# Optimization experiments

Hardware: AMD Instinct MI355X
Metric: run time of the kernel (lower is better)

Reference implementation:

```python
import jax, jax.numpy as jnp
import numpy as np
from jax import lax

TAU = 1.0
GUMBEL_SCALE = 1e-4
SEARCH_SPACE = [1, 2, 4, 8, 16, 32, 64]


def synth_weight(weight, alphas_after):
    """Per-block circulant projection of weight for each block size, mixed by alphas.

    weight: [O, I, k, k]. For block size b: reshape to (q,b,p,b,k,k), rotate rows so
    each circulant diagonal aligns, mean over the block row axis, broadcast back with
    the reverse rotation, and accumulate alpha-weighted.
    """
    O, I, k, _ = weight.shape
    w = alphas_after[0] * weight  # block_size == 1 -> identity
    for idx, b in enumerate(SEARCH_SPACE[1:], start=1):
        q, p = O // b, I // b
        tmp = weight.reshape(q, b, p, b, k, k).transpose(0, 2, 1, 3, 4, 5)  # q,p,b,b,k,k
        ii = jnp.arange(b)[:, None]
        jj = jnp.arange(b)[None, :]
        rot = tmp[:, :, ii, (ii + jj) % b]          # q,p,b,b,k,k : rotate_mat gather
        cir = rot.mean(axis=2)                       # q,p,b,k,k   : circulant mean
        out = cir[:, :, (jj - ii) % b]               # q,p,b,b,k,k : rev_rotate_mat gather
        out = out.transpose(0, 2, 1, 3, 4, 5).reshape(O, I, k, k)
        w = w + alphas_after[idx] * out
    return w


def setup_inputs() -> dict:
    key = jax.random.key(0)
    k1, k2, k3 = jax.random.split(key, 3)
    B, C, H = 16, 256, 56
    O, I, K = 256, 256, 3
    x = jax.random.normal(k1, (B, C, H, H), dtype=jnp.float32)
    # kaiming-uniform-ish init: uniform in [-bound, bound], bound = sqrt(6/fan_in)
    fan_in = I * K * K
    bound = float(np.sqrt(6.0 / fan_in))
    weight = jax.random.uniform(k2, (O, I, K, K), dtype=jnp.float32, minval=-bound, maxval=bound)
    alphas = jnp.ones((len(SEARCH_SPACE),), dtype=jnp.float32)
    gumbels = jax.random.normal(k3, (len(SEARCH_SPACE),), dtype=jnp.float32)
    return {"x": x, "weight": weight, "alphas": alphas, "gumbels": gumbels}


def reference(x, weight, alphas, gumbels):
    # gumbel_softmax with tiny Gumbel(0, 1e-4) noise (noise passed in for determinism)
    alphas_after = jax.nn.softmax((alphas + GUMBEL_SCALE * gumbels) / TAU, axis=-1)
    w = synth_weight(weight, alphas_after)
    k = weight.shape[-1]
    pad = k // 2
    stride = 1
    out = lax.conv_general_dilated(
        x, w,
        window_strides=(stride, stride),
        padding=[(pad, pad), (pad, pad)],
        dimension_numbers=("NCHW", "OIHW", "NCHW"),
    )
    return out
```

## Files before the change

kernel.cpp:

```cpp
#include <hip/hip_runtime.h>
#include <hip/hip_bf16.h>

typedef __attribute__((ext_vector_type(8))) short bf16x8;
typedef __attribute__((ext_vector_type(4))) float f32x4;

#define WR_OFF   27557888

#define BAND 24576

__global__ void diagsum_kernel(const float* __restrict__ W, float* __restrict__ S) {
    int t = blockIdx.x * 256 + threadIdx.x;
    int idx, n, lvlOff;
    if (t < 32768)      { idx = 1; n = t;          lvlOff = 0; }
    else if (t < 49152) { idx = 2; n = t - 32768;  lvlOff = 294912; }
    else if (t < 57344) { idx = 3; n = t - 49152;  lvlOff = 442368; }
    else if (t < 61440) { idx = 4; n = t - 57344;  lvlOff = 516096; }
    else if (t < 63488) { idx = 5; n = t - 61440;  lvlOff = 552960; }
    else                { idx = 6; n = t - 63488;  lvlOff = 571392; }
    int b = 1 << idx;
    int d = n & (b - 1);
    int qp = n >> idx;
    int p = qp & ((256 >> idx) - 1);
    int q = qp >> (8 - idx);
    float s[9];
    #pragma unroll
    for (int tp = 0; tp < 9; ++tp) s[tp] = 0.f;
    for (int tt = 0; tt < b; ++tt) {
        const float* wp = W + ((size_t)((q * b + tt) * 256 + p * b + ((tt + d) & (b - 1)))) * 9;
        #pragma unroll
        for (int tp = 0; tp < 9; ++tp) s[tp] += wp[tp];
    }
    float* o = S + (size_t)lvlOff + (size_t)n * 9;
    #pragma unroll
    for (int tp = 0; tp < 9; ++tp) o[tp] = s[tp];
}

__global__ void wsynth_kernel(const float* __restrict__ W,
                              const float* __restrict__ alphas,
                              const float* __restrict__ gumbels,
                              const float* __restrict__ S,
                              __hip_bfloat16* __restrict__ Wr) {
    int tid = blockIdx.x * 256 + threadIdx.x;
    int o = tid >> 8, i = tid & 255;

    float a[7]; float mx = -1e30f;
    for (int j = 0; j < 7; ++j) { a[j] = alphas[j] + 1.0e-4f * gumbels[j]; mx = fmaxf(mx, a[j]); }
    float s = 0.f;
    for (int j = 0; j < 7; ++j) { a[j] = __expf(a[j] - mx); s += a[j]; }
    float invs = 1.0f / s;
    for (int j = 0; j < 7; ++j) a[j] *= invs;

    float acc[9];
    const float* w0 = W + ((size_t)(o * 256 + i)) * 9;
    #pragma unroll
    for (int t = 0; t < 9; ++t) acc[t] = a[0] * w0[t];

    const int lvlOff[7] = {0, 0, 294912, 442368, 516096, 552960, 571392};
    int dif = i - o;
    #pragma unroll
    for (int idx = 1; idx < 7; ++idx) {
        int b = 1 << idx;
        int q = o >> idx, p = i >> idx, d = dif & (b - 1);
        int n = ((q * (256 >> idx) + p) << idx) + d;
        const float* sp = S + lvlOff[idx] + (size_t)n * 9;
        float sc = a[idx] / (float)b;
        #pragma unroll
        for (int tp = 0; tp < 9; ++tp) acc[tp] += sc * sp[tp];
    }
    const size_t eb = (size_t)(i >> 5) * 8192 + ((i >> 3) & 3) * 2048 + o * 8 + (i & 7);
    #pragma unroll
    for (int tp = 0; tp < 9; ++tp)
        Wr[(size_t)tp * 65536 + eb] = __float2bfloat16(acc[tp]);
}

__global__ void pad_nhwc_kernel(const float* __restrict__ x,
                                __hip_bfloat16* __restrict__ Xp) {
    {
        int bl = (blockIdx.z * 4 + blockIdx.y) * 49 + blockIdx.x;
        int L = bl * 256 + threadIdx.x;
        for (int e = L; e < 933888; e += 802816) {
            int c = e & 255;
            int pp = e >> 8;
            int b = pp / 228;
            int p = pp - b * 228;
            int y, xx;
            if (p < 58)       { y = 0;             xx = p; }
            else if (p < 116) { y = 57;            xx = p - 58; }
            else if (p < 172) { y = 1 + (p - 116); xx = 0; }
            else              { y = 1 + (p - 172); xx = 57; }
            Xp[((size_t)(b * 58 + y) * 58 + xx) * 256 + c] = __float2bfloat16(0.f);
        }
    }
    __shared__ float t[64][65];
    int p0 = blockIdx.x * 64;
    int c0 = blockIdx.y * 64;
    int b  = blockIdx.z;
    int lane = threadIdx.x & 63;
    int grp  = threadIdx.x >> 6;

    const float* src = x + ((size_t)(b * 256 + c0)) * 3136 + p0;
    #pragma unroll
    for (int it = 0; it < 16; ++it) {
        int c = it * 4 + grp;
        t[c][lane] = src[(size_t)c * 3136 + lane];
    }
    __syncthreads();
    #pragma unroll
    for (int it = 0; it < 16; ++it) {
        int pl = it * 4 + grp;
        int P = p0 + pl;
        int y = P / 56, xx = P - y * 56;
        Xp[(((size_t)(b * 58 + y + 1)) * 58 + (xx + 1)) * 256 + c0 + lane] =
            __float2bfloat16(t[lane][pl]);
    }
}

__device__ __forceinline__ void gload16(const __hip_bfloat16* g, char* l) {
    __builtin_amdgcn_global_load_lds(
        (const __attribute__((address_space(1))) void*)g,
        (__attribute__((address_space(3))) void*)l, 16, 0, 0);
}

template<int N> __device__ __forceinline__ void gate() {
    if constexpr (N == 0)      asm volatile("s_waitcnt vmcnt(0)" ::: "memory");
    else if constexpr (N == 4) asm volatile("s_waitcnt vmcnt(4)" ::: "memory");
}

template<bool LAST>
__device__ __forceinline__ void chunk_pair(
    int cp, char* smem, const char* aBase,
    const int (&bOff)[7], const __hip_bfloat16* const (&xSrc)[3],
    int tid, bf16x8 (&afr)[2][4], bf16x8 (&bfv)[2][7], f32x4 (&acc)[4][7])
{
    #pragma unroll
    for (int u = 0; u < 2; ++u) {
        const int cc = 2 * cp + u;
        const char* xb = smem + u * BAND;
        #pragma unroll
        for (int r = 0; r < 9; ++r) {
            const int cur = (u + r) & 1, nxt = cur ^ 1;
            if (r == 0 && !(LAST && u == 1)) {
                char* d = smem + (u ^ 1) * BAND + tid * 16;
                #pragma unroll
                for (int it = 0; it < 3; ++it)
                    gload16(xSrc[it] + (cc + 1) * 32, d + it * 8192);
            }
            if (!(LAST && u == 1 && r == 8)) {
                const int tapn = (r == 8) ? 0 : r + 1;
                const int aoff = tapn * 131072 + (cc + (r == 8 ? 1 : 0)) * 16384;
                #pragma unroll
                for (int nf = 0; nf < 4; ++nf)
                    afr[nxt][nf] = *(const bf16x8*)(aBase + aoff + nf * 256);
            }
            if (r < 8) {
                const int tapn = r + 1;
                const int timn = ((tapn / 3 - 1) * 64 + (tapn % 3 - 1)) * 16;
                #pragma unroll
                for (int mf = 0; mf < 7; ++mf)
                    bfv[nxt][mf] = *(const bf16x8*)(xb + bOff[mf] + timn);
            } else if (!(LAST && u == 1)) {
                const int timn = (-64 - 1) * 16;
                const char* xb2 = smem + (u ^ 1) * BAND;
                #pragma unroll
                for (int mf = 0; mf < 7; ++mf)
                    bfv[nxt][mf] = *(const bf16x8*)(xb2 + bOff[mf] + timn);
            }
            __builtin_amdgcn_sched_barrier(0);
            __builtin_amdgcn_s_setprio(1);
            #pragma unroll
            for (int nf = 0; nf < 4; ++nf)
                #pragma unroll
                for (int mf = 0; mf < 7; ++mf)
                    acc[nf][mf] = __builtin_amdgcn_mfma_f32_16x16x32_bf16(
                        afr[cur][nf], bfv[cur][mf], acc[nf][mf], 0, 0, 0);
            __builtin_amdgcn_s_setprio(0);
            if (r == 7 && !(LAST && u == 1)) {
                gate<4>();
                __builtin_amdgcn_s_barrier();
            }
        }
    }
}

__global__ __launch_bounds__(512, 2) void conv_kernel(
        const __hip_bfloat16* __restrict__ Xp,
        const __hip_bfloat16* __restrict__ Wr,
        float* __restrict__ out) {
    __shared__ char smem[2 * BAND];

    const int tid = threadIdx.x;
    const int w = tid >> 6, lane = tid & 63, l15 = lane & 15, q = lane >> 4;
    const int bid = blockIdx.x;
    const int bimg = bid / 14;
    const int y0 = (bid - bimg * 14) * 4;

    const int wn = (w & 3) << 6;
    const int wm = (w >> 2) * 112;

    const char* aBase = (const char*)Wr + q * 4096 + (wn + l15) * 16;

    const __hip_bfloat16* xSrc[3];
    #pragma unroll
    for (int it = 0; it < 3; ++it) {
        int chunk = tid + it * 512;
        int slot = chunk / 384;
        int rem  = chunk - slot * 384;
        int row = rem >> 6, xcol = rem & 63;
        xSrc[it] = Xp + (((size_t)(bimg * 58 + y0 + row)) * 58 + xcol) * 256 + slot * 8;
    }

    int bOff[7];
    #pragma unroll
    for (int mf = 0; mf < 7; ++mf) {
        int p = wm + mf * 16 + l15;
        int y = p / 56, xx = p - y * 56;
        bOff[mf] = q * 6144 + ((y + 1) * 64 + (xx + 1)) * 16;
    }

    f32x4 acc[4][7];
    #pragma unroll
    for (int a1 = 0; a1 < 4; ++a1)
        #pragma unroll
        for (int a2 = 0; a2 < 7; ++a2)
            acc[a1][a2] = (f32x4){0.f, 0.f, 0.f, 0.f};

    bf16x8 afr[2][4], bfv[2][7];

    {
        char* d = smem + tid * 16;
        #pragma unroll
        for (int it = 0; it < 3; ++it) gload16(xSrc[it], d + it * 8192);
    }
    #pragma unroll
    for (int nf = 0; nf < 4; ++nf)
        afr[0][nf] = *(const bf16x8*)(aBase + nf * 256);
    gate<0>();
    __builtin_amdgcn_s_barrier();
    {
        const int timm = (-64 - 1) * 16;
        #pragma unroll
        for (int mf = 0; mf < 7; ++mf)
            bfv[0][mf] = *(const bf16x8*)(smem + bOff[mf] + timm);
    }

    for (int cp = 0; cp < 3; ++cp)
        chunk_pair<false>(cp, smem, aBase, bOff, xSrc, tid, afr, bfv, acc);
    chunk_pair<true>(3, smem, aBase, bOff, xSrc, tid, afr, bfv, acc);

    const int nb = wn + q * 4;
    const size_t obB = (size_t)bimg * 256 * 3136;
    #pragma unroll
    for (int mf = 0; mf < 7; ++mf) {
        int pm = y0 * 56 + wm + mf * 16 + l15;
        #pragma unroll
        for (int nf = 0; nf < 4; ++nf) {
            #pragma unroll
            for (int rr = 0; rr < 4; ++rr)
                out[obB + (size_t)(nb + nf * 16 + rr) * 3136 + pm] = acc[nf][mf][rr];
        }
    }
}

extern "C" void kernel_launch(void* const* d_in, const int* in_sizes, int n_in,
                              void* d_out, int out_size, void* d_ws, size_t ws_size,
                              hipStream_t stream) {
    const float* x       = (const float*)d_in[0];
    const float* weight  = (const float*)d_in[1];
    const float* alphas  = (const float*)d_in[2];
    const float* gumbels = (const float*)d_in[3];
    float* out = (float*)d_out;

    __hip_bfloat16* Xp = (__hip_bfloat16*)d_ws;
    float*          S  = (float*)d_ws;
    __hip_bfloat16* Wr = (__hip_bfloat16*)((char*)d_ws + WR_OFF);

    hipLaunchKernelGGL(diagsum_kernel,  dim3(252),       dim3(256), 0, stream,
                       weight, S);
    hipLaunchKernelGGL(wsynth_kernel,   dim3(256),       dim3(256), 0, stream,
                       weight, alphas, gumbels, S, Wr);
    hipLaunchKernelGGL(pad_nhwc_kernel, dim3(49, 4, 16), dim3(256), 0, stream,
                       x, Xp);
    hipLaunchKernelGGL(conv_kernel,     dim3(224),       dim3(512), 0, stream,
                       Xp, Wr, out);
}
```

Before: 96.57 us.

## Merge diagsum and pad kernels into one prep launch, drop MFMA priority hints

Folds the diagonal-sum kernel and the input pad/NHWC transpose kernel into a single launch whose block index selects the role. The diagonal-sum scratch buffer moves from the workspace to the output buffer so it no longer overlaps the padded input. This cuts one launch and lets the two independent prep stages run side by side. It also removes the sched_barrier and setprio calls around the MFMA loop in the conv kernel, which may change instruction interleaving.

```diff
diff --git a/kernel.cpp b/kernel.cpp
--- a/kernel.cpp
+++ b/kernel.cpp
@@ -8,76 +8,41 @@
 
 #define BAND 24576
 
-__global__ void diagsum_kernel(const float* __restrict__ W, float* __restrict__ S) {
-    int t = blockIdx.x * 256 + threadIdx.x;
-    int idx, n, lvlOff;
-    if (t < 32768)      { idx = 1; n = t;          lvlOff = 0; }
-    else if (t < 49152) { idx = 2; n = t - 32768;  lvlOff = 294912; }
-    else if (t < 57344) { idx = 3; n = t - 49152;  lvlOff = 442368; }
-    else if (t < 61440) { idx = 4; n = t - 57344;  lvlOff = 516096; }
-    else if (t < 63488) { idx = 5; n = t - 61440;  lvlOff = 552960; }
-    else                { idx = 6; n = t - 63488;  lvlOff = 571392; }
-    int b = 1 << idx;
-    int d = n & (b - 1);
-    int qp = n >> idx;
-    int p = qp & ((256 >> idx) - 1);
-    int q = qp >> (8 - idx);
-    float s[9];
-    #pragma unroll
-    for (int tp = 0; tp < 9; ++tp) s[tp] = 0.f;
-    for (int tt = 0; tt < b; ++tt) {
-        const float* wp = W + ((size_t)((q * b + tt) * 256 + p * b + ((tt + d) & (b - 1)))) * 9;
-        #pragma unroll
-        for (int tp = 0; tp < 9; ++tp) s[tp] += wp[tp];
-    }
-    float* o = S + (size_t)lvlOff + (size_t)n * 9;
-    #pragma unroll
-    for (int tp = 0; tp < 9; ++tp) o[tp] = s[tp];
-}
-
-__global__ void wsynth_kernel(const float* __restrict__ W,
-                              const float* __restrict__ alphas,
-                              const float* __restrict__ gumbels,
-                              const float* __restrict__ S,
-                              __hip_bfloat16* __restrict__ Wr) {
-    int tid = blockIdx.x * 256 + threadIdx.x;
-    int o = tid >> 8, i = tid & 255;
-
-    float a[7]; float mx = -1e30f;
-    for (int j = 0; j < 7; ++j) { a[j] = alphas[j] + 1.0e-4f * gumbels[j]; mx = fmaxf(mx, a[j]); }
-    float s = 0.f;
-    for (int j = 0; j < 7; ++j) { a[j] = __expf(a[j] - mx); s += a[j]; }
-    float invs = 1.0f / s;
-    for (int j = 0; j < 7; ++j) a[j] *= invs;
-
-    float acc[9];
-    const float* w0 = W + ((size_t)(o * 256 + i)) * 9;
-    #pragma unroll
-    for (int t = 0; t < 9; ++t) acc[t] = a[0] * w0[t];
-
-    const int lvlOff[7] = {0, 0, 294912, 442368, 516096, 552960, 571392};
-    int dif = i - o;
-    #pragma unroll
-    for (int idx = 1; idx < 7; ++idx) {
+__global__ void prep_kernel(const float* __restrict__ W, float* __restrict__ S,
+                            const float* __restrict__ x,
+                            __hip_bfloat16* __restrict__ Xp) {
+    __shared__ float t[64][65];
+    if (blockIdx.x < 252) {
+        int tt = blockIdx.x * 256 + threadIdx.x;
+        int idx, n, lvlOff;
+        if (tt < 32768)      { idx = 1; n = tt;          lvlOff = 0; }
+        else if (tt < 49152) { idx = 2; n = tt - 32768;  lvlOff = 294912; }
+        else if (tt < 57344) { idx = 3; n = tt - 49152;  lvlOff = 442368; }
+        else if (tt < 61440) { idx = 4; n = tt - 57344;  lvlOff = 516096; }
+        else if (tt < 63488) { idx = 5; n = tt - 61440;  lvlOff = 552960; }
+        else                 { idx = 6; n = tt - 63488;  lvlOff = 571392; }
         int b = 1 << idx;
-        int q = o >> idx, p = i >> idx, d = dif & (b - 1);
-        int n = ((q * (256 >> idx) + p) << idx) + d;
-        const float* sp = S + lvlOff[idx] + (size_t)n * 9;
-        float sc = a[idx] / (float)b;
-        #pragma unroll
-        for (int tp = 0; tp < 9; ++tp) acc[tp] += sc * sp[tp];
-    }
-    const size_t eb = (size_t)(i >> 5) * 8192 + ((i >> 3) & 3) * 2048 + o * 8 + (i & 7);
-    #pragma unroll
-    for (int tp = 0; tp < 9; ++tp)
-        Wr[(size_t)tp * 65536 + eb] = __float2bfloat16(acc[tp]);
-}
-
-__global__ void pad_nhwc_kernel(const float* __restrict__ x,
-                                __hip_bfloat16* __restrict__ Xp) {
+        int d = n & (b - 1);
+        int qp = n >> idx;
+        int p = qp & ((256 >> idx) - 1);
+        int q = qp >> (8 - idx);
+        float s[9];
+        #pragma unroll
+        for (int tp = 0; tp < 9; ++tp) s[tp] = 0.f;
+        for (int ti = 0; ti < b; ++ti) {
+            const float* wp = W + ((size_t)((q * b + ti) * 256 + p * b + ((ti + d) & (b - 1)))) * 9;
+            #pragma unroll
+            for (int tp = 0; tp < 9; ++tp) s[tp] += wp[tp];
+        }
+        float* o = S + (size_t)lvlOff + (size_t)n * 9;
+        #pragma unroll
+        for (int tp = 0; tp < 9; ++tp) o[tp] = s[tp];
+        return;
+    }
+    int bl = blockIdx.x - 252;
+    int bx = bl % 49, by = (bl / 49) % 4, bz = bl / 196;
     {
-        int bl = (blockIdx.z * 4 + blockIdx.y) * 49 + blockIdx.x;
-        int L = bl * 256 + threadIdx.x;
+        int L = ((bz * 4 + by) * 49 + bx) * 256 + threadIdx.x;
         for (int e = L; e < 933888; e += 802816) {
             int c = e & 255;
             int pp = e >> 8;
@@ -91,10 +56,9 @@
             Xp[((size_t)(b * 58 + y) * 58 + xx) * 256 + c] = __float2bfloat16(0.f);
         }
     }
-    __shared__ float t[64][65];
-    int p0 = blockIdx.x * 64;
-    int c0 = blockIdx.y * 64;
-    int b  = blockIdx.z;
+    int p0 = bx * 64;
+    int c0 = by * 64;
+    int b  = bz;
     int lane = threadIdx.x & 63;
     int grp  = threadIdx.x >> 6;
 
@@ -115,6 +79,44 @@
     }
 }
 
+__global__ void wsynth_kernel(const float* __restrict__ W,
+                              const float* __restrict__ alphas,
+                              const float* __restrict__ gumbels,
+                              const float* __restrict__ S,
+                              __hip_bfloat16* __restrict__ Wr) {
+    int tid = blockIdx.x * 256 + threadIdx.x;
+    int o = tid >> 8, i = tid & 255;
+
+    float a[7]; float mx = -1e30f;
+    for (int j = 0; j < 7; ++j) { a[j] = alphas[j] + 1.0e-4f * gumbels[j]; mx = fmaxf(mx, a[j]); }
+    float s = 0.f;
+    for (int j = 0; j < 7; ++j) { a[j] = __expf(a[j] - mx); s += a[j]; }
+    float invs = 1.0f / s;
+    for (int j = 0; j < 7; ++j) a[j] *= invs;
+
+    float acc[9];
+    const float* w0 = W + ((size_t)(o * 256 + i)) * 9;
+    #pragma unroll
+    for (int t = 0; t < 9; ++t) acc[t] = a[0] * w0[t];
+
+    const int lvlOff[7] = {0, 0, 294912, 442368, 516096, 552960, 571392};
+    int dif = i - o;
+    #pragma unroll
+    for (int idx = 1; idx < 7; ++idx) {
+        int b = 1 << idx;
+        int q = o >> idx, p = i >> idx, d = dif & (b - 1);
+        int n = ((q * (256 >> idx) + p) << idx) + d;
+        const float* sp = S + lvlOff[idx] + (size_t)n * 9;
+        float sc = a[idx] / (float)b;
+        #pragma unroll
+        for (int tp = 0; tp < 9; ++tp) acc[tp] += sc * sp[tp];
+    }
+    const size_t eb = (size_t)(i >> 5) * 8192 + ((i >> 3) & 3) * 2048 + o * 8 + (i & 7);
+    #pragma unroll
+    for (int tp = 0; tp < 9; ++tp)
+        Wr[(size_t)tp * 65536 + eb] = __float2bfloat16(acc[tp]);
+}
+
 __device__ __forceinline__ void gload16(const __hip_bfloat16* g, char* l) {
     __builtin_amdgcn_global_load_lds(
         (const __attribute__((address_space(1))) void*)g,
@@ -165,15 +167,12 @@
                 for (int mf = 0; mf < 7; ++mf)
                     bfv[nxt][mf] = *(const bf16x8*)(xb2 + bOff[mf] + timn);
             }
-            __builtin_amdgcn_sched_barrier(0);
-            __builtin_amdgcn_s_setprio(1);
             #pragma unroll
             for (int nf = 0; nf < 4; ++nf)
                 #pragma unroll
                 for (int mf = 0; mf < 7; ++mf)
                     acc[nf][mf] = __builtin_amdgcn_mfma_f32_16x16x32_bf16(
                         afr[cur][nf], bfv[cur][mf], acc[nf][mf], 0, 0, 0);
-            __builtin_amdgcn_s_setprio(0);
             if (r == 7 && !(LAST && u == 1)) {
                 gate<4>();
                 __builtin_amdgcn_s_barrier();
@@ -271,15 +270,13 @@
     float* out = (float*)d_out;
 
     __hip_bfloat16* Xp = (__hip_bfloat16*)d_ws;
-    float*          S  = (float*)d_ws;
     __hip_bfloat16* Wr = (__hip_bfloat16*)((char*)d_ws + WR_OFF);
-
-    hipLaunchKernelGGL(diagsum_kernel,  dim3(252),       dim3(256), 0, stream,
-                       weight, S);
-    hipLaunchKernelGGL(wsynth_kernel,   dim3(256),       dim3(256), 0, stream,
+    float*          S  = (float*)d_out;
+
+    hipLaunchKernelGGL(prep_kernel,   dim3(3388), dim3(256), 0, stream,
+                       weight, S, x, Xp);
+    hipLaunchKernelGGL(wsynth_kernel, dim3(256),  dim3(256), 0, stream,
                        weight, alphas, gumbels, S, Wr);
-    hipLaunchKernelGGL(pad_nhwc_kernel, dim3(49, 4, 16), dim3(256), 0, stream,
-                       x, Xp);
-    hipLaunchKernelGGL(conv_kernel,     dim3(224),       dim3(512), 0, stream,
+    hipLaunchKernelGGL(conv_kernel,   dim3(224),  dim3(512), 0, stream,
                        Xp, Wr, out);
 }
```

Result: no change. 98.44 us (+1.9%).
